# Performance work log

Hardware: AMD Instinct MI355X
Metric: run time of the kernel (lower is better)

The kernel has to match this reference:

```python
import jax, jax.numpy as jnp
import numpy as np

B, L, D, H, E, K = 16, 197, 768, 12, 8, 2
HID = 4 * D
HD = D // H
SCALE = HD ** -0.5
EPS = 1e-5


def _layernorm(x, g, b):
    m = jnp.mean(x, axis=-1, keepdims=True)
    v = jnp.mean((x - m) ** 2, axis=-1, keepdims=True)
    return (x - m) * jax.lax.rsqrt(v + EPS) * g + b


def setup_inputs() -> dict:
    key = jax.random.key(0)
    ks = jax.random.split(key, 8)
    s = 0.02
    return {
        "x": jax.random.normal(ks[0], (B, L, D), jnp.float32),
        "ln1_g": jnp.ones((D,), jnp.float32),
        "ln1_b": jnp.zeros((D,), jnp.float32),
        "qkv_w": jax.random.normal(ks[1], (D, 3 * D), jnp.float32) * s,
        "qkv_b": jnp.zeros((3 * D,), jnp.float32),
        "proj_w": jax.random.normal(ks[2], (D, D), jnp.float32) * s,
        "proj_b": jnp.zeros((D,), jnp.float32),
        "ln2_g": jnp.ones((D,), jnp.float32),
        "ln2_b": jnp.zeros((D,), jnp.float32),
        "w_gate": jax.random.normal(ks[3], (D, E), jnp.float32) * s,
        "w1": jax.random.normal(ks[4], (E, D, HID), jnp.float32) * s,
        "b1": jnp.zeros((E, HID), jnp.float32),
        "w2": jax.random.normal(ks[5], (E, HID, D), jnp.float32) * s,
        "b2": jnp.zeros((E, D), jnp.float32),
    }


def reference(x, ln1_g, ln1_b, qkv_w, qkv_b, proj_w, proj_b,
              ln2_g, ln2_b, w_gate, w1, b1, w2, b2):
    # --- attention branch: x = x + attn(norm1(x)) ---
    h = _layernorm(x, ln1_g, ln1_b)
    qkv = (h @ qkv_w + qkv_b).reshape(B, L, 3, H, HD)
    q, k, v = [qkv[:, :, i].transpose(0, 2, 1, 3) for i in range(3)]  # [B,H,L,HD]
    attn = jax.nn.softmax(jnp.einsum('bhqd,bhkd->bhqk', q, k) * SCALE, axis=-1)
    o = jnp.einsum('bhqk,bhkd->bhqd', attn, v).transpose(0, 2, 1, 3).reshape(B, L, D)
    x = x + o @ proj_w + proj_b

    # --- MoE FFN branch on norm2(x), tokens flattened ---
    flat = _layernorm(x, ln2_g, ln2_b).reshape(-1, D)  # [T, D], T = B*L
    T = flat.shape[0]
    # noisy top-k gating, eval path (no noise): top-(k+1) logits, softmax over top-k
    logits = flat @ w_gate                              # [T, E]
    top_vals, top_idx = jax.lax.top_k(logits, K + 1)
    probs = jax.nn.softmax(top_vals[:, :K], axis=-1)    # [T, K]
    gates = jnp.zeros((T, E), flat.dtype).at[
        jnp.arange(T)[:, None], top_idx[:, :K]].set(probs)  # sparse gate matrix

    # dense equivalent of SparseDispatcher dispatch -> expert MLP -> combine:
    # output[t] = sum_e gates[t,e] * (gelu(flat @ w1[e] + b1[e]) @ w2[e] + b2[e])
    hid = jax.nn.gelu(jnp.einsum('td,edf->tef', flat, w1) + b1, approximate=False)
    y = jnp.einsum('te,tef,efd->td', gates, hid, w2) + gates @ b2
    return x + y.reshape(B, L, D)
```

## Files before the change

kernel.cpp:

```cpp
#include <hip/hip_runtime.h>
#include <math.h>
#include <stdint.h>

typedef unsigned short u16;
typedef unsigned int u32;
typedef float floatx4 __attribute__((ext_vector_type(4)));
typedef __bf16 bf16x8 __attribute__((ext_vector_type(8)));

#define T_TOK 3152
#define SEQ 197
#define NH 12
#define LISTN 7424
#define MOE_MT 58

__device__ __forceinline__ float bf2f(u16 u) { return __uint_as_float(((u32)u) << 16); }
__device__ __forceinline__ u16 f2bf(float f) {
    u32 u = __float_as_uint(f);
    u += 0x7FFFu + ((u >> 16) & 1u);
    return (u16)(u >> 16);
}
__device__ __forceinline__ float wred_sum(float v) {
#pragma unroll
    for (int off = 32; off; off >>= 1) v += __shfl_xor(v, off);
    return v;
}

__device__ __forceinline__ float gelu_fast(float v) {
    float x = fabsf(v) * 0.70710678118654752f;
    float t = __builtin_amdgcn_rcpf(fmaf(0.3275911f, x, 1.0f));
    float p = t * fmaf(t, fmaf(t, fmaf(t, fmaf(t, 1.061405429f, -1.453152027f),
                                       1.421413741f), -0.284496736f), 0.254829592f);
    float er = fmaf(-p, __expf(-x * x), 1.0f);
    er = copysignf(er, v);
    return 0.5f * v * (1.0f + er);
}

#define GLB_AS(p) ((const __attribute__((address_space(1))) void*)(uintptr_t)(p))
#define LDS_AS(p) ((__attribute__((address_space(3))) void*)(uintptr_t)(p))
__device__ __forceinline__ void gl_lds16(const u16* g, u16* l) {
    __builtin_amdgcn_global_load_lds(GLB_AS(g), LDS_AS(l), 16, 0, 0);
}

template <int SPLIT>
__global__ __launch_bounds__(256) void transp_kernel(const float* __restrict__ in,
        u16* __restrict__ oh, u16* __restrict__ ol, int R, int C) {
    int r0 = blockIdx.x * 64, c0 = blockIdx.y * 64;
    size_t zo = (size_t)blockIdx.z * R * C;
    __shared__ float Lt[64][68];
    int tid = threadIdx.x;
    int rr = tid >> 2, cs = (tid & 3) * 16;
    const float* src = in + zo + (size_t)(r0 + rr) * C + c0 + cs;
#pragma unroll
    for (int i = 0; i < 4; i++) *(float4*)&Lt[rr][cs + i * 4] = *(const float4*)(src + i * 4);
    __syncthreads();
    int cw = tid >> 2, rs = (tid & 3) * 16;
    u16 hv[16], lv[16];
#pragma unroll
    for (int j = 0; j < 16; j++) {
        float v = Lt[rs + j][cw];
        u16 hb = f2bf(v);
        hv[j] = hb;
        if (SPLIT) lv[j] = f2bf(v - bf2f(hb));
    }
    u16* dst = oh + zo + (size_t)(c0 + cw) * R + r0 + rs;
    *(uint4*)dst = *(const uint4*)&hv[0];
    *(uint4*)(dst + 8) = *(const uint4*)&hv[8];
    if (SPLIT) {
        u16* dstl = ol + zo + (size_t)(c0 + cw) * R + r0 + rs;
        *(uint4*)dstl = *(const uint4*)&lv[0];
        *(uint4*)(dstl + 8) = *(const uint4*)&lv[8];
    }
}

__global__ __launch_bounds__(256) void ln1_kernel(const float* __restrict__ x,
        const float* __restrict__ g, const float* __restrict__ b,
        u16* __restrict__ h_hi, u16* __restrict__ h_lo) {
    int t = blockIdx.x, tid = threadIdx.x;
    int w = tid >> 6, lane = tid & 63;
    float v[3];
#pragma unroll
    for (int i = 0; i < 3; i++) v[i] = x[(size_t)t * 768 + tid + i * 256];
    float s = v[0] + v[1] + v[2];
    float q = v[0] * v[0] + v[1] * v[1] + v[2] * v[2];
    s = wred_sum(s); q = wred_sum(q);
    __shared__ float red[8];
    if (lane == 0) { red[w] = s; red[4 + w] = q; }
    __syncthreads();
    float st = red[0] + red[1] + red[2] + red[3];
    float qt = red[4] + red[5] + red[6] + red[7];
    float mean = st * (1.f / 768.f);
    float var = qt * (1.f / 768.f) - mean * mean;
    float rs = rsqrtf(var + 1e-5f);
#pragma unroll
    for (int i = 0; i < 3; i++) {
        int d = tid + i * 256;
        float hv = (v[i] - mean) * rs * g[d] + b[d];
        u16 hi = f2bf(hv);
        h_hi[(size_t)t * 768 + d] = hi;
        h_lo[(size_t)t * 768 + d] = f2bf(hv - bf2f(hi));
    }
}

template <int MODE>
__global__ __launch_bounds__(256) void gemm128(const u16* __restrict__ Ah,
        const u16* __restrict__ Al, const u16* __restrict__ Bh, const u16* __restrict__ Bl,
        const float* __restrict__ bias, void* __restrict__ Cv, void* __restrict__ Cv2,
        const float* __restrict__ resid,
        const int* __restrict__ list, const int* __restrict__ asg, int M, int N, int K) {
    constexpr bool SPLIT = (MODE <= 1);
    constexpr int GX = (MODE <= 1) ? 25 : MOE_MT;
    constexpr int GY = (MODE == 0) ? 18 : (MODE == 2) ? 24 : 6;
    constexpr int GZ = (MODE == 3) ? 2 : 1;
    constexpr int G  = GX * GY * GZ;
    constexpr int NT = GY * GZ;
    constexpr int Q8 = G >> 3, R8 = G & 7;

    int d = blockIdx.x + GX * (blockIdx.y + GY * blockIdx.z);
    int j = d & 7, s = d >> 3;
    int v = (j < R8) ? (j * (Q8 + 1) + s) : (R8 * (Q8 + 1) + (j - R8) * Q8 + s);
    int mt = v / NT, nzr = v - mt * NT;
    int yt = nzr % GY, zt = nzr / GY;
    int m0 = mt * 128, n0 = yt * 128;

    const u16* Bph = Bh;
    const float* bp = bias;
    const u16* Bpl = Bl;
    if (MODE >= 2) {
        if (m0 >= asg[8]) return;
        int e = 0;
        while (m0 >= asg[e + 1]) ++e;
        Bph = Bh + (size_t)e * N * K;
        bp = bias + (size_t)e * N;
    }
    int kbeg = 0, kend = K;
    if (MODE == 3) { int kh = K >> 1; kbeg = zt * kh; kend = kbeg + kh; }

    __shared__ __align__(16) u16 SM[SPLIT ? 32768 : 24576];
    u16* Ash = SM;
    u16* Bsh = SM + (SPLIT ? 8192 : 12288);
    u16* Asl = SM + 16384;
    u16* Bsl = SM + 24576;

    int tid = threadIdx.x;
    int w = tid >> 6, lane = tid & 63, l15 = lane & 15, quad = lane >> 4;
    int wm = (w & 1) * 64, wn = (w >> 1) * 64;
    int lr = lane >> 2;
    int lc = ((lane & 3) ^ ((lane >> 3) & 3)) * 8;

    const u16* ga[2]; const u16* gal[2];
    const u16* gb[2]; const u16* gbl[2];
    int ldro[2];
#pragma unroll
    for (int it = 0; it < 2; it++) {
        int arow = m0 + it * 64 + w * 16 + lr;
        if (MODE == 2) {
            int entry = list[arow];
            ga[it] = Ah + (size_t)(entry >= 0 ? (entry >> 1) : 0) * K + lc;
        } else if (MODE == 3) {
            ga[it] = Ah + (size_t)arow * K + lc;
        } else {
            int rc = min(arow, M - 1);
            ga[it] = Ah + (size_t)rc * K + lc;
            gal[it] = Al + (size_t)rc * K + lc;
        }
        int brow = n0 + it * 64 + w * 16 + lr;
        gb[it] = Bph + (size_t)brow * K + lc;
        if (SPLIT) gbl[it] = Bpl + (size_t)brow * K + lc;
        ldro[it] = (it * 64 + w * 16) * 32;
    }

    int ra[4], rb[4];
#pragma unroll
    for (int i = 0; i < 4; i++) {
        int r1 = wm + i * 16 + l15;
        ra[i] = r1 * 32 + (quad ^ ((r1 >> 1) & 3)) * 8;
        int r2 = wn + i * 16 + l15;
        rb[i] = r2 * 32 + (quad ^ ((r2 >> 1) & 3)) * 8;
    }

    floatx4 acc[4][4];
#pragma unroll
    for (int mi = 0; mi < 4; mi++)
#pragma unroll
        for (int ni = 0; ni < 4; ni++) acc[mi][ni] = (floatx4){0.f, 0.f, 0.f, 0.f};

    auto stage = [&](int buf, int k0) {
        int bo = buf * 4096;
#pragma unroll
        for (int it = 0; it < 2; it++) {
            gl_lds16(ga[it] + k0, &Ash[bo + ldro[it]]);
            gl_lds16(gb[it] + k0, &Bsh[bo + ldro[it]]);
            if constexpr (SPLIT) {
                gl_lds16(gal[it] + k0, &Asl[bo + ldro[it]]);
                gl_lds16(gbl[it] + k0, &Bsl[bo + ldro[it]]);
            }
        }
    };
    auto compute = [&](int buf) {
        int bo = buf * 4096;
        bf16x8 afh[4], bfh[4], afl[4], bfl[4];
#pragma unroll
        for (int i = 0; i < 4; i++) {
            afh[i] = *(const bf16x8*)&Ash[bo + ra[i]];
            bfh[i] = *(const bf16x8*)&Bsh[bo + rb[i]];
            if constexpr (SPLIT) {
                afl[i] = *(const bf16x8*)&Asl[bo + ra[i]];
                bfl[i] = *(const bf16x8*)&Bsl[bo + rb[i]];
            }
        }
        __builtin_amdgcn_s_setprio(1);
#pragma unroll
        for (int mi = 0; mi < 4; mi++)
#pragma unroll
            for (int ni = 0; ni < 4; ni++) {
                if constexpr (SPLIT) {
                    acc[mi][ni] = __builtin_amdgcn_mfma_f32_16x16x32_bf16(afl[mi], bfh[ni], acc[mi][ni], 0, 0, 0);
                    acc[mi][ni] = __builtin_amdgcn_mfma_f32_16x16x32_bf16(afh[mi], bfl[ni], acc[mi][ni], 0, 0, 0);
                }
                acc[mi][ni] = __builtin_amdgcn_mfma_f32_16x16x32_bf16(afh[mi], bfh[ni], acc[mi][ni], 0, 0, 0);
            }
        __builtin_amdgcn_s_setprio(0);
    };

    int nsteps = (kend - kbeg) >> 5;
    if constexpr (SPLIT) {
        stage(0, kbeg);
        stage(1, kbeg + 32);
        asm volatile("s_waitcnt vmcnt(8)" ::: "memory");
        __builtin_amdgcn_s_barrier();
        for (int t = 0; t < nsteps; ++t) {
            compute(t & 1);
            asm volatile("s_waitcnt lgkmcnt(0)" ::: "memory");
            __builtin_amdgcn_s_barrier();
            if (t + 2 < nsteps) {
                stage(t & 1, kbeg + (t + 2) * 32);
                asm volatile("s_waitcnt vmcnt(8)" ::: "memory");
            } else if (t + 1 < nsteps) {
                asm volatile("s_waitcnt vmcnt(0)" ::: "memory");
            }
        }
    } else {
        stage(0, kbeg);
        stage(1, kbeg + 32);
        asm volatile("s_waitcnt vmcnt(4)" ::: "memory");
        __builtin_amdgcn_s_barrier();
        int bufc = 0;
        for (int t = 0; t < nsteps; ++t) {
            int b2 = bufc + 2; if (b2 >= 3) b2 -= 3;
            if (t + 2 < nsteps) stage(b2, kbeg + (t + 2) * 32);
            compute(bufc);
            if (t + 2 < nsteps) {
                asm volatile("s_waitcnt vmcnt(4) lgkmcnt(0)" ::: "memory");
            } else {
                asm volatile("s_waitcnt vmcnt(0) lgkmcnt(0)" ::: "memory");
            }
            __builtin_amdgcn_s_barrier();
            bufc = (bufc == 2) ? 0 : bufc + 1;
        }
    }

    if constexpr (MODE == 2) {
#pragma unroll
        for (int ni = 0; ni < 4; ni++) {
            int col = wn + ni * 16 + l15;
            float bb = bp[n0 + col];
#pragma unroll
            for (int mi = 0; mi < 4; mi++) {
#pragma unroll
                for (int r = 0; r < 4; r++) {
                    int row = wm + mi * 16 + quad * 4 + r;
                    float gv = gelu_fast(acc[mi][ni][r] + bb);
                    SM[row * 128 + (col ^ ((row & 7) << 3))] = f2bf(gv);
                }
            }
        }
        __syncthreads();
        int rr = tid >> 1, half = (tid & 1) * 64;
        int grow = m0 + rr;
        if (list[grow] >= 0) {
            u16* dst = (u16*)Cv + (size_t)grow * N + n0 + half;
            int xr = (rr & 7) << 3;
#pragma unroll
            for (int gch = 0; gch < 8; gch++) {
                int cb = (half + gch * 8) ^ xr;
                *(uint4*)(dst + gch * 8) = *(const uint4*)&SM[rr * 128 + cb];
            }
        }
        return;
    }

    float* Cf = (float*)Cv;
    if (MODE == 3 && zt != 0) Cf = (float*)Cv2;
#pragma unroll
    for (int ni = 0; ni < 4; ni++) {
        int col = n0 + wn + ni * 16 + l15;
        float bb = bp[col];
        if (MODE == 3 && zt != 0) bb = 0.f;
#pragma unroll
        for (int mi = 0; mi < 4; mi++) {
#pragma unroll
            for (int r = 0; r < 4; r++) {
                int row = m0 + wm + mi * 16 + quad * 4 + r;
                float v2 = acc[mi][ni][r] + bb;
                if (MODE == 0) {
                    if (row < M) {
                        u16 hb = f2bf(v2);
                        ((u16*)Cv)[(size_t)row * N + col] = hb;
                        ((u16*)Cv2)[(size_t)row * N + col] = f2bf(v2 - bf2f(hb));
                    }
                } else if (MODE == 1) {
                    if (row < M) Cf[(size_t)row * N + col] = v2 + resid[(size_t)row * N + col];
                } else {
                    if (list[row] >= 0) Cf[(size_t)row * N + col] = v2;
                }
            }
        }
    }
}

__global__ __launch_bounds__(256) void attn_mfma_kernel(const u16* __restrict__ qph,
        const u16* __restrict__ qpl, u16* __restrict__ ohi, u16* __restrict__ olo) {
    int d = blockIdx.x + 4 * blockIdx.y;
    int j = d & 7, sdx = d >> 3;
    int v = j * 96 + sdx;
    int qbase = (v & 3) * 64;
    int by = v >> 2;
    int b = by / NH, h = by % NH;
    int tid = threadIdx.x;
    int w = tid >> 6, lane = tid & 63, l15 = lane & 15, quad = lane >> 4;

    __shared__ u16 Qh[64 * 64], Ql[64 * 64];
    __shared__ u16 Sh[64 * 64], Sl[64 * 64];
    __shared__ u16 Ph[64 * 72], Pl[64 * 72];

    int grow8 = lane >> 3;
    int gsrc = ((lane & 7) ^ grow8) * 8;
    int srow = tid >> 2;
    int scol = (tid & 3) * 16;

#pragma unroll
    for (int it = 0; it < 2; it++) {
        int r = qbase + w * 16 + it * 8 + grow8;
        int rc = min(r, SEQ - 1);
        size_t so = (size_t)(b * SEQ + rc) * 2304 + h * 64 + gsrc;
        gl_lds16(qph + so, &Qh[(w * 16 + it * 8) * 64]);
        gl_lds16(qpl + so, &Ql[(w * 16 + it * 8) * 64]);
    }
    __syncthreads();
    bf16x8 aqh[2], aql[2];
#pragma unroll
    for (int s2 = 0; s2 < 2; s2++) {
        int row = w * 16 + l15;
        int ad = row * 64 + (((s2 * 4 + quad) ^ (row & 7))) * 8;
        aqh[s2] = *(const bf16x8*)&Qh[ad];
        aql[s2] = *(const bf16x8*)&Ql[ad];
    }

    floatx4 sc[16];
#pragma unroll
    for (int f = 0; f < 16; f++) sc[f] = (floatx4){0.f, 0.f, 0.f, 0.f};

    for (int t = 0; t < 4; t++) {
#pragma unroll
        for (int it = 0; it < 2; it++) {
            int r = t * 64 + w * 16 + it * 8 + grow8;
            int rc = min(r, SEQ - 1);
            size_t so = (size_t)(b * SEQ + rc) * 2304 + 768 + h * 64 + gsrc;
            gl_lds16(qph + so, &Sh[(w * 16 + it * 8) * 64]);
            gl_lds16(qpl + so, &Sl[(w * 16 + it * 8) * 64]);
        }
        __syncthreads();
#pragma unroll
        for (int s = 0; s < 4; s++) {
            int row = s * 16 + l15;
#pragma unroll
            for (int s2 = 0; s2 < 2; s2++) {
                int ad = row * 64 + (((s2 * 4 + quad) ^ (row & 7))) * 8;
                bf16x8 bkh = *(const bf16x8*)&Sh[ad];
                bf16x8 bkl = *(const bf16x8*)&Sl[ad];
                sc[t * 4 + s] = __builtin_amdgcn_mfma_f32_16x16x32_bf16(aql[s2], bkh, sc[t * 4 + s], 0, 0, 0);
                sc[t * 4 + s] = __builtin_amdgcn_mfma_f32_16x16x32_bf16(aqh[s2], bkl, sc[t * 4 + s], 0, 0, 0);
                sc[t * 4 + s] = __builtin_amdgcn_mfma_f32_16x16x32_bf16(aqh[s2], bkh, sc[t * 4 + s], 0, 0, 0);
            }
        }
        __syncthreads();
    }

    float m[4] = {-1e30f, -1e30f, -1e30f, -1e30f};
#pragma unroll
    for (int f = 0; f < 16; f++) {
        int key = (f >> 2) * 64 + (f & 3) * 16 + l15;
        bool valid = key < SEQ;
#pragma unroll
        for (int r = 0; r < 4; r++) {
            float s = valid ? sc[f][r] * 0.125f : -1e30f;
            sc[f][r] = s;
            m[r] = fmaxf(m[r], s);
        }
    }
#pragma unroll
    for (int r = 0; r < 4; r++) {
#pragma unroll
        for (int off = 1; off < 16; off <<= 1) m[r] = fmaxf(m[r], __shfl_xor(m[r], off));
    }
    float sum[4] = {0.f, 0.f, 0.f, 0.f};
#pragma unroll
    for (int f = 0; f < 16; f++) {
#pragma unroll
        for (int r = 0; r < 4; r++) {
            float p = expf(sc[f][r] - m[r]);
            sc[f][r] = p;
            sum[r] += p;
        }
    }
    float inv[4];
#pragma unroll
    for (int r = 0; r < 4; r++) {
#pragma unroll
        for (int off = 1; off < 16; off <<= 1) sum[r] += __shfl_xor(sum[r], off);
        inv[r] = 1.f / sum[r];
    }

    floatx4 oacc[4];
#pragma unroll
    for (int sd = 0; sd < 4; sd++) oacc[sd] = (floatx4){0.f, 0.f, 0.f, 0.f};

    for (int t = 0; t < 4; t++) {
#pragma unroll
        for (int s = 0; s < 4; s++) {
#pragma unroll
            for (int r = 0; r < 4; r++) {
                float p = sc[t * 4 + s][r];
                u16 hb = f2bf(p);
                int row = w * 16 + quad * 4 + r;
                Ph[row * 72 + s * 16 + l15] = hb;
                Pl[row * 72 + s * 16 + l15] = f2bf(p - bf2f(hb));
            }
        }
        {
            int key = t * 64 + srow;
            int kc = min(key, SEQ - 1);
            size_t so = (size_t)(b * SEQ + kc) * 2304 + 1536 + h * 64 + scol;
            u16 hv[16], lv[16];
            *(uint4*)&hv[0] = *(const uint4*)(qph + so);
            *(uint4*)&hv[8] = *(const uint4*)(qph + so + 8);
            *(uint4*)&lv[0] = *(const uint4*)(qpl + so);
            *(uint4*)&lv[8] = *(const uint4*)(qpl + so + 8);
            int kg = srow >> 3, kw = srow & 7;
#pragma unroll
            for (int i = 0; i < 16; i++) {
                int dcol = scol + i;
                int idx = dcol * 64 + ((kg ^ (dcol & 7)) * 8) + kw;
                Sh[idx] = hv[i];
                Sl[idx] = lv[i];
            }
        }
        __syncthreads();
#pragma unroll
        for (int s2 = 0; s2 < 2; s2++) {
            bf16x8 aph = *(const bf16x8*)&Ph[(w * 16 + l15) * 72 + s2 * 32 + quad * 8];
            bf16x8 apl = *(const bf16x8*)&Pl[(w * 16 + l15) * 72 + s2 * 32 + quad * 8];
#pragma unroll
            for (int sd = 0; sd < 4; sd++) {
                int row = sd * 16 + l15;
                int ad = row * 64 + (((s2 * 4 + quad) ^ (row & 7))) * 8;
                bf16x8 bvh = *(const bf16x8*)&Sh[ad];
                bf16x8 bvl = *(const bf16x8*)&Sl[ad];
                oacc[sd] = __builtin_amdgcn_mfma_f32_16x16x32_bf16(apl, bvh, oacc[sd], 0, 0, 0);
                oacc[sd] = __builtin_amdgcn_mfma_f32_16x16x32_bf16(aph, bvl, oacc[sd], 0, 0, 0);
                oacc[sd] = __builtin_amdgcn_mfma_f32_16x16x32_bf16(aph, bvh, oacc[sd], 0, 0, 0);
            }
        }
        __syncthreads();
    }

#pragma unroll
    for (int sd = 0; sd < 4; sd++) {
#pragma unroll
        for (int r = 0; r < 4; r++) {
            int q = qbase + w * 16 + quad * 4 + r;
            if (q < SEQ) {
                float val = oacc[sd][r] * inv[r];
                u16 hb = f2bf(val);
                size_t o = ((size_t)(b * SEQ + q)) * 768 + h * 64 + sd * 16 + l15;
                ohi[o] = hb;
                olo[o] = f2bf(val - bf2f(hb));
            }
        }
    }
}

__global__ __launch_bounds__(256) void ln2_gate_kernel(const float* __restrict__ x1,
        const float* __restrict__ g, const float* __restrict__ b, const float* __restrict__ wg,
        u16* __restrict__ flat, int2* __restrict__ idx, float2* __restrict__ gate,
        int* __restrict__ cnt) {
    int t = blockIdx.x, tid = threadIdx.x;
    int w = tid >> 6, lane = tid & 63;
    float v[3];
#pragma unroll
    for (int i = 0; i < 3; i++) v[i] = x1[(size_t)t * 768 + tid + i * 256];
    float s = v[0] + v[1] + v[2];
    float q = v[0] * v[0] + v[1] * v[1] + v[2] * v[2];
    s = wred_sum(s); q = wred_sum(q);
    __shared__ float red[8];
    __shared__ float fs[768];
    __shared__ float lg[8];
    if (lane == 0) { red[w] = s; red[4 + w] = q; }
    __syncthreads();
    float st = red[0] + red[1] + red[2] + red[3];
    float qt = red[4] + red[5] + red[6] + red[7];
    float mean = st * (1.f / 768.f);
    float var = qt * (1.f / 768.f) - mean * mean;
    float rs = rsqrtf(var + 1e-5f);
#pragma unroll
    for (int i = 0; i < 3; i++) {
        int d = tid + i * 256;
        float f = (v[i] - mean) * rs * g[d] + b[d];
        flat[(size_t)t * 768 + d] = f2bf(f);
        fs[d] = f;
    }
    __syncthreads();
    int e0 = 2 * w, e1 = 2 * w + 1;
    float p0 = 0.f, p1 = 0.f;
    for (int d = lane; d < 768; d += 64) {
        float f = fs[d];
        p0 += f * wg[d * 8 + e0];
        p1 += f * wg[d * 8 + e1];
    }
    p0 = wred_sum(p0); p1 = wred_sum(p1);
    if (lane == 0) { lg[e0] = p0; lg[e1] = p1; }
    __syncthreads();
    if (tid == 0) {
        float b0 = -1e30f, b1 = -1e30f;
        int i0 = 0, i1 = 0;
        for (int e = 0; e < 8; e++) {
            float le = lg[e];
            if (le > b0) { b1 = b0; i1 = i0; b0 = le; i0 = e; }
            else if (le > b1) { b1 = le; i1 = e; }
        }
        float ex = expf(b1 - b0);
        float den = 1.f + ex;
        idx[t] = make_int2(i0, i1);
        gate[t] = make_float2(1.f / den, ex / den);
        atomicAdd(&cnt[i0], 1);
        atomicAdd(&cnt[i1], 1);
    }
}

__global__ void offsets_kernel(const int* __restrict__ cnt, int* __restrict__ asg) {
    if (threadIdx.x == 0 && blockIdx.x == 0) {
        int acc = 0;
        asg[0] = 0;
        for (int e = 0; e < 8; e++) { acc += (cnt[e] + 127) & ~127; asg[e + 1] = acc; }
    }
}

__global__ __launch_bounds__(256) void scatter_kernel(const int2* __restrict__ idx,
        const int* __restrict__ asg, int* __restrict__ cursor,
        int* __restrict__ list, int* __restrict__ pos) {
    int t = blockIdx.x * 256 + threadIdx.x;
    if (t >= T_TOK) return;
    int2 id = idx[t];
    int p0 = asg[id.x] + atomicAdd(&cursor[id.x], 1);
    list[p0] = t * 2;
    pos[t * 2] = p0;
    int p1 = asg[id.y] + atomicAdd(&cursor[id.y], 1);
    list[p1] = t * 2 + 1;
    pos[t * 2 + 1] = p1;
}

__global__ __launch_bounds__(256) void final_kernel(const float* __restrict__ x1,
        const float* __restrict__ yp0, const float* __restrict__ yp1, const int* __restrict__ pos,
        const float2* __restrict__ gate, float* __restrict__ out) {
    int t = blockIdx.x, tid = threadIdx.x;
    float2 g = gate[t];
    int p0 = pos[t * 2], p1 = pos[t * 2 + 1];
#pragma unroll
    for (int i = 0; i < 3; i++) {
        int d = tid + i * 256;
        float y0 = yp0[(size_t)p0 * 768 + d] + yp1[(size_t)p0 * 768 + d];
        float y1 = yp0[(size_t)p1 * 768 + d] + yp1[(size_t)p1 * 768 + d];
        out[(size_t)t * 768 + d] = x1[(size_t)t * 768 + d] + g.x * y0 + g.y * y1;
    }
}

extern "C" void kernel_launch(void* const* d_in, const int* in_sizes, int n_in,
                              void* d_out, int out_size, void* d_ws, size_t ws_size,
                              hipStream_t stream) {
    const float* x      = (const float*)d_in[0];
    const float* ln1_g  = (const float*)d_in[1];
    const float* ln1_b  = (const float*)d_in[2];
    const float* qkv_w  = (const float*)d_in[3];
    const float* qkv_b  = (const float*)d_in[4];
    const float* proj_w = (const float*)d_in[5];
    const float* proj_b = (const float*)d_in[6];
    const float* ln2_g  = (const float*)d_in[7];
    const float* ln2_b  = (const float*)d_in[8];
    const float* w_gate = (const float*)d_in[9];
    const float* w1     = (const float*)d_in[10];
    const float* b1     = (const float*)d_in[11];
    const float* w2     = (const float*)d_in[12];
    const float* b2     = (const float*)d_in[13];

    char* ws = (char*)d_ws;
    size_t off = 0;
    auto alloc = [&](size_t bytes) { size_t cur = off; off = (off + bytes + 255) & ~(size_t)255; return cur; };
    u16*    h_hi   = (u16*)   (ws + alloc((size_t)T_TOK * 768 * 2));
    u16*    h_lo   = (u16*)   (ws + alloc((size_t)T_TOK * 768 * 2));
    u16*    qkv_hi = (u16*)   (ws + alloc((size_t)T_TOK * 2304 * 2));
    u16*    qkv_lo = (u16*)   (ws + alloc((size_t)T_TOK * 2304 * 2));
    u16*    o_hi   = (u16*)   (ws + alloc((size_t)T_TOK * 768 * 2));
    u16*    o_lo   = (u16*)   (ws + alloc((size_t)T_TOK * 768 * 2));
    float*  ypair0 = (float*) ws;
    float*  x1     = (float*) (ws + alloc((size_t)T_TOK * 768 * 4));
    u16*    flat   = (u16*)   (ws + alloc((size_t)T_TOK * 768 * 2));
    int2*   idx    = (int2*)  (ws + alloc((size_t)T_TOK * 8));
    float2* gate   = (float2*)(ws + alloc((size_t)T_TOK * 8));
    int*    cnt    = (int*)   (ws + alloc(64));
    int*    cursor = cnt + 8;
    int*    asg    = (int*)   (ws + alloc(64));
    int*    list   = (int*)   (ws + alloc((size_t)LISTN * 4));
    int*    pos    = (int*)   (ws + alloc((size_t)T_TOK * 2 * 4));
    u16*    hid    = (u16*)   (ws + alloc((size_t)LISTN * 3072 * 2));
    u16*    qkvt_h = (u16*)   (ws + alloc((size_t)2304 * 768 * 2));
    u16*    qkvt_l = (u16*)   (ws + alloc((size_t)2304 * 768 * 2));
    u16*    projt_h = (u16*)  (ws + alloc((size_t)768 * 768 * 2));
    u16*    projt_l = (u16*)  (ws + alloc((size_t)768 * 768 * 2));
    u16*    w1t    = (u16*)   (ws + alloc((size_t)8 * 3072 * 768 * 2));
    u16*    w2t    = (u16*)   (ws + alloc((size_t)8 * 768 * 3072 * 2));
    float*  ypair1 = (float*) w1t;

    hipMemsetAsync(cnt, 0, 64, stream);
    hipMemsetAsync(list, 0xFF, (size_t)LISTN * 4, stream);

    transp_kernel<1><<<dim3(12, 36, 1), 256, 0, stream>>>(qkv_w, qkvt_h, qkvt_l, 768, 2304);
    transp_kernel<1><<<dim3(12, 12, 1), 256, 0, stream>>>(proj_w, projt_h, projt_l, 768, 768);
    transp_kernel<0><<<dim3(12, 48, 8), 256, 0, stream>>>(w1, w1t, nullptr, 768, 3072);
    transp_kernel<0><<<dim3(48, 12, 8), 256, 0, stream>>>(w2, w2t, nullptr, 3072, 768);

    ln1_kernel<<<T_TOK, 256, 0, stream>>>(x, ln1_g, ln1_b, h_hi, h_lo);
    gemm128<0><<<dim3(25, 18), 256, 0, stream>>>(h_hi, h_lo, qkvt_h, qkvt_l, qkv_b, qkv_hi,
                                                 qkv_lo, nullptr, nullptr, nullptr, T_TOK, 2304, 768);
    attn_mfma_kernel<<<dim3(4, 192), 256, 0, stream>>>(qkv_hi, qkv_lo, o_hi, o_lo);
    gemm128<1><<<dim3(25, 6), 256, 0, stream>>>(o_hi, o_lo, projt_h, projt_l, proj_b, x1,
                                                nullptr, x, nullptr, nullptr, T_TOK, 768, 768);
    ln2_gate_kernel<<<T_TOK, 256, 0, stream>>>(x1, ln2_g, ln2_b, w_gate, flat, idx, gate, cnt);
    offsets_kernel<<<1, 64, 0, stream>>>(cnt, asg);
    scatter_kernel<<<(T_TOK + 255) / 256, 256, 0, stream>>>(idx, asg, cursor, list, pos);
    gemm128<2><<<dim3(MOE_MT, 24), 256, 0, stream>>>(flat, nullptr, w1t, nullptr, b1, hid,
                                                     nullptr, nullptr, list, asg, LISTN, 3072, 768);
    gemm128<3><<<dim3(MOE_MT, 6, 2), 256, 0, stream>>>(hid, nullptr, w2t, nullptr, b2, ypair0,
                                                       ypair1, nullptr, list, asg, LISTN, 768, 3072);
    final_kernel<<<T_TOK, 256, 0, stream>>>(x1, ypair0, ypair1, pos, gate, (float*)d_out);
}
```

Measured before the change: 583.7 us.

## Use one wave per token in LN2 gating and fuse MoE routing into one kernel

The LN2+gate kernel now gives each token a single wavefront using float4 loads, so the LDS reductions and block barriers go away. It reads a pre-transposed gate weight for coalesced logits. The global atomic counts, offsets kernel and scatter kernel are replaced by a single-block route kernel that counts per expert and assigns deterministic positions with ballot/popcount prefix sums. This cuts kernel launches and atomics, but the routing now runs serially on one workgroup.

```diff
diff --git a/kernel.cpp b/kernel.cpp
--- a/kernel.cpp
+++ b/kernel.cpp
@@ -20,6 +20,11 @@
     return (u16)(u >> 16);
 }
 __device__ __forceinline__ float wred_sum(float v) {
+#pragma unroll
+    for (int off = 32; off; off >>= 1) v += __shfl_xor(v, off);
+    return v;
+}
+__device__ __forceinline__ int wred_sum_i(int v) {
 #pragma unroll
     for (int off = 32; off; off >>= 1) v += __shfl_xor(v, off);
     return v;
@@ -450,9 +455,9 @@
 #pragma unroll
             for (int i = 0; i < 16; i++) {
                 int dcol = scol + i;
-                int idx = dcol * 64 + ((kg ^ (dcol & 7)) * 8) + kw;
-                Sh[idx] = hv[i];
-                Sl[idx] = lv[i];
+                int idx2 = dcol * 64 + ((kg ^ (dcol & 7)) * 8) + kw;
+                Sh[idx2] = hv[i];
+                Sl[idx2] = lv[i];
             }
         }
         __syncthreads();
@@ -490,49 +495,68 @@
     }
 }
 
+__global__ void wgt_kernel(const float* __restrict__ wg, float* __restrict__ wgT) {
+    for (int i = threadIdx.x; i < 768 * 8; i += 256) {
+        int d = i >> 3, e = i & 7;
+        wgT[e * 768 + d] = wg[i];
+    }
+}
+
 __global__ __launch_bounds__(256) void ln2_gate_kernel(const float* __restrict__ x1,
-        const float* __restrict__ g, const float* __restrict__ b, const float* __restrict__ wg,
-        u16* __restrict__ flat, int2* __restrict__ idx, float2* __restrict__ gate,
-        int* __restrict__ cnt) {
-    int t = blockIdx.x, tid = threadIdx.x;
-    int w = tid >> 6, lane = tid & 63;
-    float v[3];
-#pragma unroll
-    for (int i = 0; i < 3; i++) v[i] = x1[(size_t)t * 768 + tid + i * 256];
-    float s = v[0] + v[1] + v[2];
-    float q = v[0] * v[0] + v[1] * v[1] + v[2] * v[2];
+        const float* __restrict__ g, const float* __restrict__ b, const float* __restrict__ wgT,
+        u16* __restrict__ flat, int2* __restrict__ idx, float2* __restrict__ gate) {
+    int w = threadIdx.x >> 6, lane = threadIdx.x & 63;
+    int t = blockIdx.x * 4 + w;
+    if (t >= T_TOK) return;
+    const float* xp = x1 + (size_t)t * 768;
+    float v[3][4];
+    float s = 0.f, q = 0.f;
+#pragma unroll
+    for (int i = 0; i < 3; i++) {
+        float4 f4 = *(const float4*)(xp + i * 256 + lane * 4);
+        v[i][0] = f4.x; v[i][1] = f4.y; v[i][2] = f4.z; v[i][3] = f4.w;
+#pragma unroll
+        for (int j2 = 0; j2 < 4; j2++) { s += v[i][j2]; q += v[i][j2] * v[i][j2]; }
+    }
     s = wred_sum(s); q = wred_sum(q);
-    __shared__ float red[8];
-    __shared__ float fs[768];
-    __shared__ float lg[8];
-    if (lane == 0) { red[w] = s; red[4 + w] = q; }
-    __syncthreads();
-    float st = red[0] + red[1] + red[2] + red[3];
-    float qt = red[4] + red[5] + red[6] + red[7];
-    float mean = st * (1.f / 768.f);
-    float var = qt * (1.f / 768.f) - mean * mean;
+    float mean = s * (1.f / 768.f);
+    float var = q * (1.f / 768.f) - mean * mean;
     float rs = rsqrtf(var + 1e-5f);
+    float fs[3][4];
 #pragma unroll
     for (int i = 0; i < 3; i++) {
-        int d = tid + i * 256;
-        float f = (v[i] - mean) * rs * g[d] + b[d];
-        flat[(size_t)t * 768 + d] = f2bf(f);
-        fs[d] = f;
-    }
-    __syncthreads();
-    int e0 = 2 * w, e1 = 2 * w + 1;
-    float p0 = 0.f, p1 = 0.f;
-    for (int d = lane; d < 768; d += 64) {
-        float f = fs[d];
-        p0 += f * wg[d * 8 + e0];
-        p1 += f * wg[d * 8 + e1];
-    }
-    p0 = wred_sum(p0); p1 = wred_sum(p1);
-    if (lane == 0) { lg[e0] = p0; lg[e1] = p1; }
-    __syncthreads();
-    if (tid == 0) {
+        int d0 = i * 256 + lane * 4;
+        float4 g4 = *(const float4*)(g + d0);
+        float4 b4 = *(const float4*)(b + d0);
+        float gg[4] = {g4.x, g4.y, g4.z, g4.w};
+        float bb[4] = {b4.x, b4.y, b4.z, b4.w};
+        u16 hv[4];
+#pragma unroll
+        for (int j2 = 0; j2 < 4; j2++) {
+            float f = (v[i][j2] - mean) * rs * gg[j2] + bb[j2];
+            fs[i][j2] = f;
+            hv[j2] = f2bf(f);
+        }
+        *(uint2*)&flat[(size_t)t * 768 + d0] = *(const uint2*)hv;
+    }
+    float lg[8];
+#pragma unroll
+    for (int e = 0; e < 8; e++) {
+        float p = 0.f;
+#pragma unroll
+        for (int i = 0; i < 3; i++) {
+            float4 wv = *(const float4*)(wgT + e * 768 + i * 256 + lane * 4);
+            p = fmaf(fs[i][0], wv.x, p);
+            p = fmaf(fs[i][1], wv.y, p);
+            p = fmaf(fs[i][2], wv.z, p);
+            p = fmaf(fs[i][3], wv.w, p);
+        }
+        lg[e] = wred_sum(p);
+    }
+    if (lane == 0) {
         float b0 = -1e30f, b1 = -1e30f;
         int i0 = 0, i1 = 0;
+#pragma unroll
         for (int e = 0; e < 8; e++) {
             float le = lg[e];
             if (le > b0) { b1 = b0; i1 = i0; b0 = le; i0 = e; }
@@ -542,31 +566,75 @@
         float den = 1.f + ex;
         idx[t] = make_int2(i0, i1);
         gate[t] = make_float2(1.f / den, ex / den);
-        atomicAdd(&cnt[i0], 1);
-        atomicAdd(&cnt[i1], 1);
-    }
-}
-
-__global__ void offsets_kernel(const int* __restrict__ cnt, int* __restrict__ asg) {
-    if (threadIdx.x == 0 && blockIdx.x == 0) {
+    }
+}
+
+__global__ __launch_bounds__(256) void route_kernel(const int2* __restrict__ idx,
+        int* __restrict__ asg, int* __restrict__ list, int* __restrict__ pos) {
+    int tid = threadIdx.x, w = tid >> 6, lane = tid & 63;
+    __shared__ int wcnt[4][8];
+    __shared__ int run[8];
+
+    int myc[8] = {0, 0, 0, 0, 0, 0, 0, 0};
+    for (int t = tid; t < T_TOK; t += 256) {
+        int2 id = idx[t];
+#pragma unroll
+        for (int e = 0; e < 8; e++) myc[e] += (id.x == e) + (id.y == e);
+    }
+#pragma unroll
+    for (int e = 0; e < 8; e++) {
+        int c = wred_sum_i(myc[e]);
+        if (lane == 0) wcnt[w][e] = c;
+    }
+    __syncthreads();
+    if (tid == 0) {
         int acc = 0;
-        asg[0] = 0;
-        for (int e = 0; e < 8; e++) { acc += (cnt[e] + 127) & ~127; asg[e + 1] = acc; }
-    }
-}
-
-__global__ __launch_bounds__(256) void scatter_kernel(const int2* __restrict__ idx,
-        const int* __restrict__ asg, int* __restrict__ cursor,
-        int* __restrict__ list, int* __restrict__ pos) {
-    int t = blockIdx.x * 256 + threadIdx.x;
-    if (t >= T_TOK) return;
-    int2 id = idx[t];
-    int p0 = asg[id.x] + atomicAdd(&cursor[id.x], 1);
-    list[p0] = t * 2;
-    pos[t * 2] = p0;
-    int p1 = asg[id.y] + atomicAdd(&cursor[id.y], 1);
-    list[p1] = t * 2 + 1;
-    pos[t * 2 + 1] = p1;
+        for (int e = 0; e < 8; e++) {
+            run[e] = acc;
+            asg[e] = acc;
+            int c = wcnt[0][e] + wcnt[1][e] + wcnt[2][e] + wcnt[3][e];
+            acc += (c + 127) & ~127;
+        }
+        asg[8] = acc;
+    }
+    __syncthreads();
+
+    unsigned long long lt = (1ull << lane) - 1ull;
+    for (int c0 = 0; c0 < T_TOK; c0 += 256) {
+        int t = c0 + tid;
+        bool valid = t < T_TOK;
+        int ex = valid ? idx[t].x : -1;
+        int ey = valid ? idx[t].y : -1;
+        int rkx = 0, rky = 0;
+        int wtot[8];
+#pragma unroll
+        for (int e = 0; e < 8; e++) {
+            unsigned long long mx = __ballot(ex == e);
+            unsigned long long my = __ballot(ey == e);
+            int r = __popcll(mx & lt) + __popcll(my & lt);
+            if (ex == e) rkx = r;
+            if (ey == e) rky = r;
+            wtot[e] = __popcll(mx) + __popcll(my);
+        }
+        if (lane == 0) {
+#pragma unroll
+            for (int e = 0; e < 8; e++) wcnt[w][e] = wtot[e];
+        }
+        __syncthreads();
+        if (valid) {
+            int wpx = 0, wpy = 0;
+            for (int w2 = 0; w2 < w; w2++) { wpx += wcnt[w2][ex]; wpy += wcnt[w2][ey]; }
+            int p0 = run[ex] + wpx + rkx;
+            int p1 = run[ey] + wpy + rky;
+            list[p0] = t * 2;
+            pos[t * 2] = p0;
+            list[p1] = t * 2 + 1;
+            pos[t * 2 + 1] = p1;
+        }
+        __syncthreads();
+        if (tid < 8) run[tid] += wcnt[0][tid] + wcnt[1][tid] + wcnt[2][tid] + wcnt[3][tid];
+        __syncthreads();
+    }
 }
 
 __global__ __launch_bounds__(256) void final_kernel(const float* __restrict__ x1,
@@ -616,8 +684,7 @@
     u16*    flat   = (u16*)   (ws + alloc((size_t)T_TOK * 768 * 2));
     int2*   idx    = (int2*)  (ws + alloc((size_t)T_TOK * 8));
     float2* gate   = (float2*)(ws + alloc((size_t)T_TOK * 8));
-    int*    cnt    = (int*)   (ws + alloc(64));
-    int*    cursor = cnt + 8;
+    float*  wgT    = (float*) (ws + alloc((size_t)8 * 768 * 4));
     int*    asg    = (int*)   (ws + alloc(64));
     int*    list   = (int*)   (ws + alloc((size_t)LISTN * 4));
     int*    pos    = (int*)   (ws + alloc((size_t)T_TOK * 2 * 4));
@@ -630,13 +697,13 @@
     u16*    w2t    = (u16*)   (ws + alloc((size_t)8 * 768 * 3072 * 2));
     float*  ypair1 = (float*) w1t;
 
-    hipMemsetAsync(cnt, 0, 64, stream);
     hipMemsetAsync(list, 0xFF, (size_t)LISTN * 4, stream);
 
     transp_kernel<1><<<dim3(12, 36, 1), 256, 0, stream>>>(qkv_w, qkvt_h, qkvt_l, 768, 2304);
     transp_kernel<1><<<dim3(12, 12, 1), 256, 0, stream>>>(proj_w, projt_h, projt_l, 768, 768);
     transp_kernel<0><<<dim3(12, 48, 8), 256, 0, stream>>>(w1, w1t, nullptr, 768, 3072);
     transp_kernel<0><<<dim3(48, 12, 8), 256, 0, stream>>>(w2, w2t, nullptr, 3072, 768);
+    wgt_kernel<<<1, 256, 0, stream>>>(w_gate, wgT);
 
     ln1_kernel<<<T_TOK, 256, 0, stream>>>(x, ln1_g, ln1_b, h_hi, h_lo);
     gemm128<0><<<dim3(25, 18), 256, 0, stream>>>(h_hi, h_lo, qkvt_h, qkvt_l, qkv_b, qkv_hi,
@@ -644,9 +711,8 @@
     attn_mfma_kernel<<<dim3(4, 192), 256, 0, stream>>>(qkv_hi, qkv_lo, o_hi, o_lo);
     gemm128<1><<<dim3(25, 6), 256, 0, stream>>>(o_hi, o_lo, projt_h, projt_l, proj_b, x1,
                                                 nullptr, x, nullptr, nullptr, T_TOK, 768, 768);
-    ln2_gate_kernel<<<T_TOK, 256, 0, stream>>>(x1, ln2_g, ln2_b, w_gate, flat, idx, gate, cnt);
-    offsets_kernel<<<1, 64, 0, stream>>>(cnt, asg);
-    scatter_kernel<<<(T_TOK + 255) / 256, 256, 0, stream>>>(idx, asg, cursor, list, pos);
+    ln2_gate_kernel<<<T_TOK / 4, 256, 0, stream>>>(x1, ln2_g, ln2_b, wgT, flat, idx, gate);
+    route_kernel<<<1, 256, 0, stream>>>(idx, asg, list, pos);
     gemm128<2><<<dim3(MOE_MT, 24), 256, 0, stream>>>(flat, nullptr, w1t, nullptr, b1, hid,
                                                      nullptr, nullptr, list, asg, LISTN, 3072, 768);
     gemm128<3><<<dim3(MOE_MT, 6, 2), 256, 0, stream>>>(hid, nullptr, w2t, nullptr, b2, ypair0,
```

Result: faster. 500.8 us (-14.2%).
